# Kernel optimization log

Hardware: AMD Instinct MI355X
Metric: run time of the kernel (lower is better)

The kernel has to match this reference:

```python
import jax, jax.numpy as jnp
import numpy as np

C_CURV = 1.0   # Poincare ball curvature c
EPS = 1e-7
KERNEL = 4
STRIDE = 4


def setup_inputs() -> dict:
    key = jax.random.key(0)
    B, C, L = 16, 256, 16384
    v = jax.random.normal(key, (B, C, L), dtype=jnp.float32)
    # Project channel vectors into the Poincare ball (norm along man_dim=1 < 1)
    n = jnp.linalg.norm(v, axis=1, keepdims=True)
    x = 0.7 * v / (1.0 + n)
    return {"x": x}


def reference(x):
    # x: (B, C, L); manifold dim is axis 1 (man_dim=1)
    k, s = KERNEL, STRIDE
    B, C, L = x.shape
    out_len = (L - k) // s + 1
    # unfold along length: (out_len, k) gather indices
    idx = jnp.arange(out_len)[:, None] * s + jnp.arange(k)[None, :]
    w = x[:, :, idx]                                  # (B, C, out_len, k)
    c = C_CURV
    # Poincare -> Klein model
    x2 = jnp.sum(w * w, axis=1, keepdims=True)        # (B,1,out_len,k)
    xK = 2.0 * w / (1.0 + c * x2)
    # Lorentz factors in Klein model
    gam = 1.0 / jnp.sqrt(jnp.clip(1.0 - c * jnp.sum(xK * xK, axis=1, keepdims=True), EPS))
    # weighted Klein midpoint over the kernel window (last axis)
    mK = jnp.sum(gam * xK, axis=-1) / jnp.sum(gam, axis=-1)   # (B, C, out_len)
    # Klein -> Poincare (gyromidpoint)
    mK2 = jnp.sum(mK * mK, axis=1, keepdims=True)
    m = mK / (1.0 + jnp.sqrt(jnp.clip(1.0 - c * mK2, EPS)))
    return m
```

## Files before the change

kernel.cpp:

```cpp
#include <hip/hip_runtime.h>
#include <stdint.h>

#define B_    16
#define C_    256
#define L_    16384
#define OL_   4096
#define OT    16
#define TL    64
#define PITCH 68

__global__ __launch_bounds__(256)
void havgpool_hyp_kernel(const float* __restrict__ x, float* __restrict__ out) {
    __shared__ float tile[C_ * PITCH];
    __shared__ float p2[16 * TL];
    __shared__ float sA1[TL];
    __shared__ float sW[4 * OT];
    __shared__ float sInvm[OT];

    const int t     = threadIdx.x;
    const int otile = blockIdx.x;
    const int b     = blockIdx.y;
    const int l0    = otile * TL;
    const int o0    = otile * OT;

    const int j     = t & 15;
    const int rbase = t >> 4;

    float acc[4] = {0.f, 0.f, 0.f, 0.f};
    const float* src = x + ((size_t)b * C_ * L_ + l0 + 4 * j);
    #pragma unroll
    for (int it = 0; it < 16; ++it) {
        const int r = it * 16 + rbase;
        const float4 v = *(const float4*)(src + (size_t)r * L_);
        acc[0] += v.x * v.x;
        acc[1] += v.y * v.y;
        acc[2] += v.z * v.z;
        acc[3] += v.w * v.w;
        *(float4*)&tile[r * PITCH + 4 * j] = v;
    }
    #pragma unroll
    for (int e = 0; e < 4; ++e) p2[rbase * TL + 4 * j + e] = acc[e];

    __syncthreads();

    if (t < TL) {
        float x2 = 0.f;
        #pragma unroll
        for (int k = 0; k < 16; ++k) x2 += p2[k * TL + t];
        const float inv1 = 1.0f / (1.0f + x2);
        const float xk2  = 4.0f * x2 * inv1 * inv1;
        const float g    = rsqrtf(fmaxf(1.0f - xk2, 1e-7f));
        float G = g;
        G += __shfl_xor(G, 1, 64);
        G += __shfl_xor(G, 2, 64);
        sA1[t] = 2.0f * g * inv1 / G;
    }
    __syncthreads();

    const int c = t;
    float mK[OT];
    #pragma unroll
    for (int o = 0; o < OT; ++o) {
        const float4 v = *(const float4*)&tile[c * PITCH + 4 * o];
        mK[o] = v.x * sA1[4*o] + v.y * sA1[4*o+1] + v.z * sA1[4*o+2] + v.w * sA1[4*o+3];
    }

    const int lane = t & 63;
    const int w    = t >> 6;
    #pragma unroll
    for (int o = 0; o < OT; ++o) {
        float v = mK[o] * mK[o];
        #pragma unroll
        for (int off = 32; off >= 1; off >>= 1) v += __shfl_xor(v, off, 64);
        if (lane == o) sW[w * OT + o] = v;
    }
    __syncthreads();
    if (t < OT) {
        const float m2 = sW[t] + sW[OT + t] + sW[2 * OT + t] + sW[3 * OT + t];
        sInvm[t] = 1.0f / (1.0f + sqrtf(fmaxf(1.0f - m2, 1e-7f)));
    }
    __syncthreads();

    float* op = out + ((size_t)(b * C_ + c) * OL_ + o0);
    #pragma unroll
    for (int q = 0; q < 4; ++q) {
        float4 ov;
        ov.x = mK[4*q + 0] * sInvm[4*q + 0];
        ov.y = mK[4*q + 1] * sInvm[4*q + 1];
        ov.z = mK[4*q + 2] * sInvm[4*q + 2];
        ov.w = mK[4*q + 3] * sInvm[4*q + 3];
        *(float4*)(op + 4 * q) = ov;
    }
}

extern "C" void kernel_launch(void* const* d_in, const int* in_sizes, int n_in,
                              void* d_out, int out_size, void* d_ws, size_t ws_size,
                              hipStream_t stream) {
    const float* x = (const float*)d_in[0];
    float* out = (float*)d_out;
    dim3 grid(OL_ / OT, B_);
    havgpool_hyp_kernel<<<grid, 256, 0, stream>>>(x, out);
}
```

Before: 386.1 us.

## Keep loaded tile in registers instead of LDS and compute midpoints per load thread

Removes the 68KB shared-memory tile. Each thread keeps its 16 float4 loads in registers and computes the window midpoint directly from them. Partial norms are reduced with wave shuffles rather than a 16-row LDS array. The LDS reduction scratch shrinks, and a min-blocks-per-SM launch bound is added to raise occupancy. The trade-off is that output stores become scalar 4-byte writes strided by channel rather than float4 per channel row, which may hurt write coalescing.

```diff
diff --git a/kernel.cpp b/kernel.cpp
--- a/kernel.cpp
+++ b/kernel.cpp
@@ -7,46 +7,47 @@
 #define OL_   4096
 #define OT    16
 #define TL    64
-#define PITCH 68
 
-__global__ __launch_bounds__(256)
+__global__ __launch_bounds__(256, 4)
 void havgpool_hyp_kernel(const float* __restrict__ x, float* __restrict__ out) {
-    __shared__ float tile[C_ * PITCH];
-    __shared__ float p2[16 * TL];
+    __shared__ float sP[4][TL];
     __shared__ float sA1[TL];
-    __shared__ float sW[4 * OT];
+    __shared__ float sQ[4][OT];
     __shared__ float sInvm[OT];
 
     const int t     = threadIdx.x;
     const int otile = blockIdx.x;
     const int b     = blockIdx.y;
-    const int l0    = otile * TL;
-    const int o0    = otile * OT;
-
     const int j     = t & 15;
+    const int lane  = t & 63;
+    const int w     = t >> 6;
     const int rbase = t >> 4;
 
-    float acc[4] = {0.f, 0.f, 0.f, 0.f};
-    const float* src = x + ((size_t)b * C_ * L_ + l0 + 4 * j);
+    const float* src = x + ((size_t)b * C_ * L_ + (size_t)otile * TL + 4 * j);
+    float4 v[16];
+    float a0 = 0.f, a1 = 0.f, a2 = 0.f, a3 = 0.f;
     #pragma unroll
     for (int it = 0; it < 16; ++it) {
-        const int r = it * 16 + rbase;
-        const float4 v = *(const float4*)(src + (size_t)r * L_);
-        acc[0] += v.x * v.x;
-        acc[1] += v.y * v.y;
-        acc[2] += v.z * v.z;
-        acc[3] += v.w * v.w;
-        *(float4*)&tile[r * PITCH + 4 * j] = v;
+        v[it] = *(const float4*)(src + (size_t)(it * 16 + rbase) * L_);
+        a0 += v[it].x * v[it].x;
+        a1 += v[it].y * v[it].y;
+        a2 += v[it].z * v[it].z;
+        a3 += v[it].w * v[it].w;
     }
-    #pragma unroll
-    for (int e = 0; e < 4; ++e) p2[rbase * TL + 4 * j + e] = acc[e];
-
+    a0 += __shfl_xor(a0, 16, 64); a0 += __shfl_xor(a0, 32, 64);
+    a1 += __shfl_xor(a1, 16, 64); a1 += __shfl_xor(a1, 32, 64);
+    a2 += __shfl_xor(a2, 16, 64); a2 += __shfl_xor(a2, 32, 64);
+    a3 += __shfl_xor(a3, 16, 64); a3 += __shfl_xor(a3, 32, 64);
+    if (lane < 16) {
+        sP[w][4 * j + 0] = a0;
+        sP[w][4 * j + 1] = a1;
+        sP[w][4 * j + 2] = a2;
+        sP[w][4 * j + 3] = a3;
+    }
     __syncthreads();
 
     if (t < TL) {
-        float x2 = 0.f;
-        #pragma unroll
-        for (int k = 0; k < 16; ++k) x2 += p2[k * TL + t];
+        const float x2   = sP[0][t] + sP[1][t] + sP[2][t] + sP[3][t];
         const float inv1 = 1.0f / (1.0f + x2);
         const float xk2  = 4.0f * x2 * inv1 * inv1;
         const float g    = rsqrtf(fmaxf(1.0f - xk2, 1e-7f));
@@ -57,39 +58,31 @@
     }
     __syncthreads();
 
-    const int c = t;
-    float mK[OT];
+    const float c0 = sA1[4 * j + 0];
+    const float c1 = sA1[4 * j + 1];
+    const float c2 = sA1[4 * j + 2];
+    const float c3 = sA1[4 * j + 3];
+    float mk[16];
+    float q = 0.f;
     #pragma unroll
-    for (int o = 0; o < OT; ++o) {
-        const float4 v = *(const float4*)&tile[c * PITCH + 4 * o];
-        mK[o] = v.x * sA1[4*o] + v.y * sA1[4*o+1] + v.z * sA1[4*o+2] + v.w * sA1[4*o+3];
+    for (int it = 0; it < 16; ++it) {
+        mk[it] = v[it].x * c0 + v[it].y * c1 + v[it].z * c2 + v[it].w * c3;
+        q += mk[it] * mk[it];
     }
-
-    const int lane = t & 63;
-    const int w    = t >> 6;
-    #pragma unroll
-    for (int o = 0; o < OT; ++o) {
-        float v = mK[o] * mK[o];
-        #pragma unroll
-        for (int off = 32; off >= 1; off >>= 1) v += __shfl_xor(v, off, 64);
-        if (lane == o) sW[w * OT + o] = v;
-    }
+    q += __shfl_xor(q, 16, 64); q += __shfl_xor(q, 32, 64);
+    if (lane < 16) sQ[w][j] = q;
     __syncthreads();
     if (t < OT) {
-        const float m2 = sW[t] + sW[OT + t] + sW[2 * OT + t] + sW[3 * OT + t];
+        const float m2 = sQ[0][t] + sQ[1][t] + sQ[2][t] + sQ[3][t];
         sInvm[t] = 1.0f / (1.0f + sqrtf(fmaxf(1.0f - m2, 1e-7f)));
     }
     __syncthreads();
 
-    float* op = out + ((size_t)(b * C_ + c) * OL_ + o0);
+    const float s = sInvm[j];
+    float* op = out + (size_t)(b * C_) * OL_ + (size_t)otile * OT + j;
     #pragma unroll
-    for (int q = 0; q < 4; ++q) {
-        float4 ov;
-        ov.x = mK[4*q + 0] * sInvm[4*q + 0];
-        ov.y = mK[4*q + 1] * sInvm[4*q + 1];
-        ov.z = mK[4*q + 2] * sInvm[4*q + 2];
-        ov.w = mK[4*q + 3] * sInvm[4*q + 3];
-        *(float4*)(op + 4 * q) = ov;
+    for (int it = 0; it < 16; ++it) {
+        op[(size_t)(it * 16 + rbase) * OL_] = mk[it] * s;
     }
 }
 
```

Result: no change. 381.7 us (-1.1%).
